# Optimization experiments

Measured on AMD Instinct MI355X. Metric: run time of the kernel, lower is better.

The kernel has to match this reference:

```python
import jax, jax.numpy as jnp
import numpy as np

USER_DIM = 64
ITEM_DIM = 64
HIDDEN = 32
N_USERS = 50000
N_ITEMS = 50000
N_EDGES = 1_600_000


def _xavier_uniform(key, shape):
    fan_in, fan_out = shape[1], shape[0]
    limit = np.sqrt(6.0 / (fan_in + fan_out))
    return jax.random.uniform(key, shape, jnp.float32, -limit, limit)


def setup_inputs() -> dict:
    key = jax.random.key(0)
    k1, k2, k3, k4, k5 = jax.random.split(key, 5)
    user_embeddings = jax.random.normal(k1, (N_USERS, USER_DIM), jnp.float32)
    item_embeddings = jax.random.normal(k2, (N_ITEMS, ITEM_DIM), jnp.float32)
    edge_index = jax.random.randint(k3, (2, N_EDGES), 0, N_USERS, jnp.int64)
    # MLP params: torch Linear weight is [out, in]; xavier_uniform, zero bias
    W1 = _xavier_uniform(k4, (HIDDEN, USER_DIM + ITEM_DIM))
    b1 = jnp.zeros((HIDDEN,), jnp.float32)
    W2 = _xavier_uniform(k5, (1, HIDDEN))
    b2 = jnp.zeros((1,), jnp.float32)
    return {
        "user_embeddings": user_embeddings,
        "item_embeddings": item_embeddings,
        "W1": W1, "b1": b1, "W2": W2, "b2": b2,
        "edge_index": edge_index,
    }


def reference(user_embeddings, item_embeddings, W1, b1, W2, b2, edge_index):
    user_feats = user_embeddings[edge_index[0]]      # [E, user_dim]
    item_feats = item_embeddings[edge_index[1]]      # [E, item_dim]
    edge_feats = jnp.concatenate([user_feats, item_feats], axis=1)  # [E, user_dim+item_dim]
    h = edge_feats @ W1.T + b1                       # [E, 32]
    h = jnp.where(h >= 0, h, 0.2 * h)                # LeakyReLU(0.2)
    logits = h @ W2.T + b2                           # [E, 1]
    return jax.nn.sigmoid(logits).squeeze(-1)        # [E]
```

## Files before the change

kernel.cpp:

```cpp
#include <hip/hip_runtime.h>

typedef unsigned short ushort_t;
typedef __attribute__((ext_vector_type(8))) short short8;
typedef __attribute__((ext_vector_type(4))) float f32x4;
typedef __attribute__((ext_vector_type(2))) _Float16 h2v;
typedef __attribute__((ext_vector_type(4))) _Float16 h4v;

__device__ __forceinline__ ushort_t f2b(float x) {
    unsigned int u = __builtin_bit_cast(unsigned int, x);
    u += 0x7FFFu + ((u >> 16) & 1u);
    return (ushort_t)(u >> 16);
}

__device__ __forceinline__ short8 pack8(const float* __restrict__ p) {
    float4 f0 = *reinterpret_cast<const float4*>(p);
    float4 f1 = *reinterpret_cast<const float4*>(p + 4);
    short8 v;
    v[0] = (short)f2b(f0.x); v[1] = (short)f2b(f0.y);
    v[2] = (short)f2b(f0.z); v[3] = (short)f2b(f0.w);
    v[4] = (short)f2b(f1.x); v[5] = (short)f2b(f1.y);
    v[6] = (short)f2b(f1.z); v[7] = (short)f2b(f1.w);
    return v;
}

__global__ __launch_bounds__(256) void precompute_h(
    const float* __restrict__ ue, const float* __restrict__ ie,
    const float* __restrict__ W1, const float* __restrict__ b1,
    _Float16* __restrict__ hu, _Float16* __restrict__ hi,
    int nu, int ni, int ntu, int ntot)
{
    const int l  = threadIdx.x & 63;
    const int lj = l & 15;
    const int lg = l >> 4;

    int wid = blockIdx.x * (blockDim.x >> 6) + (threadIdx.x >> 6);
    if (wid >= ntot) return;
    const bool isU = wid < ntu;
    const float* tab = isU ? ue : ie;
    _Float16* ht = isU ? hu : hi;
    const int nrows = isU ? nu : ni;
    const int tb   = (isU ? wid : wid - ntu) * 16;
    const int toff = isU ? 0 : 64;

    short8 afrag[2][2];
#pragma unroll
    for (int ks = 0; ks < 2; ++ks)
#pragma unroll
        for (int g = 0; g < 2; ++g)
            afrag[ks][g] = pack8(W1 + (g * 16 + lj) * 128 + toff + ks * 32 + lg * 8);

    int r = tb + lj; if (r >= nrows) r = nrows - 1;
    const float* rp = tab + (long)r * 64;
    short8 bfrag0 = pack8(rp + lg * 8);
    short8 bfrag1 = pack8(rp + 32 + lg * 8);

    f32x4 acc[2];
#pragma unroll
    for (int g = 0; g < 2; ++g)
#pragma unroll
        for (int q = 0; q < 4; ++q)
            acc[g][q] = isU ? b1[g * 16 + lg * 4 + q] : 0.f;

    acc[0] = __builtin_amdgcn_mfma_f32_16x16x32_bf16(afrag[0][0], bfrag0, acc[0], 0, 0, 0);
    acc[1] = __builtin_amdgcn_mfma_f32_16x16x32_bf16(afrag[0][1], bfrag0, acc[1], 0, 0, 0);
    acc[0] = __builtin_amdgcn_mfma_f32_16x16x32_bf16(afrag[1][0], bfrag1, acc[0], 0, 0, 0);
    acc[1] = __builtin_amdgcn_mfma_f32_16x16x32_bf16(afrag[1][1], bfrag1, acc[1], 0, 0, 0);

    if (tb + lj < nrows) {
#pragma unroll
        for (int g = 0; g < 2; ++g) {
            h4v v;
#pragma unroll
            for (int q = 0; q < 4; ++q) v[q] = (_Float16)acc[g][q];
            *reinterpret_cast<h4v*>(ht + (long)r * 32 + g * 16 + lg * 4) = v;
        }
    }
}

#if __has_builtin(__builtin_amdgcn_fdot2)
__device__ __forceinline__ float fdot2(h2v a, h2v b, float c) {
    return __builtin_amdgcn_fdot2(a, b, c, false);
}
#else
__device__ __forceinline__ float fdot2(h2v a, h2v b, float c) {
    return c + (float)a[0] * (float)b[0] + (float)a[1] * (float)b[1];
}
#endif

__global__ __launch_bounds__(256) void edge_final(
    const _Float16* __restrict__ hu, const _Float16* __restrict__ hi,
    const float* __restrict__ w2, const float* __restrict__ b2v,
    const int* __restrict__ idx, float* __restrict__ out,
    long E, long ngroups)
{
    const int l = threadIdx.x & 63;
    const int c = l & 3;
    const int g = l >> 2;

    long wid = (long)blockIdx.x * (blockDim.x >> 6) + (threadIdx.x >> 6);
    if (wid >= ngroups) return;

    h2v w2h[4];
#pragma unroll
    for (int k = 0; k < 4; ++k) {
        w2h[k][0] = (_Float16)w2[c * 8 + 2 * k];
        w2h[k][1] = (_Float16)w2[c * 8 + 2 * k + 1];
    }
    const float bb2 = b2v[0];
    const _Float16 sl = (_Float16)0.2f;
    const h2v slope = {sl, sl};

    long e0 = wid * 64;
    long el = e0 + l; if (el >= E) el = E - 1;
    int uidx = idx[el];
    int iidx = idx[E + el];

    uint4 hur[4], hir[4];
#pragma unroll
    for (int s = 0; s < 4; ++s) {
        int u  = __shfl(uidx, s * 16 + g);
        int it = __shfl(iidx, s * 16 + g);
        hur[s] = *reinterpret_cast<const uint4*>(hu + (long)u  * 32 + c * 8);
        hir[s] = *reinterpret_cast<const uint4*>(hi + (long)it * 32 + c * 8);
    }

    float pt[4];
#pragma unroll
    for (int s = 0; s < 4; ++s) {
        const unsigned int* au = reinterpret_cast<const unsigned int*>(&hur[s]);
        const unsigned int* ai = reinterpret_cast<const unsigned int*>(&hir[s]);
        float p = 0.f;
#pragma unroll
        for (int k = 0; k < 4; ++k) {
            h2v a = __builtin_bit_cast(h2v, au[k]);
            h2v b = __builtin_bit_cast(h2v, ai[k]);
            h2v h = a + b;
            h = __builtin_elementwise_max(h, h * slope);
            p = fdot2(h, w2h[k], p);
        }
        p += __shfl_xor(p, 1);
        p += __shfl_xor(p, 2);
        pt[s] = p;
    }

    int src = (l & 15) * 4;
    float v0 = __shfl(pt[0], src);
    float v1 = __shfl(pt[1], src);
    float v2 = __shfl(pt[2], src);
    float v3 = __shfl(pt[3], src);
    int sr = l >> 4;
    float pv = sr == 0 ? v0 : sr == 1 ? v1 : sr == 2 ? v2 : v3;

    float x = pv + bb2;
    float z = __builtin_amdgcn_exp2f(-1.442695040888963f * x);
    float sig = __builtin_amdgcn_rcpf(1.f + z);
    long eo = e0 + l;
    if (eo < E) out[eo] = sig;
}

__global__ __launch_bounds__(256) void edge_mlp_fp32(
    const float* __restrict__ ue, const float* __restrict__ ie,
    const float* __restrict__ W1, const float* __restrict__ b1,
    const float* __restrict__ w2, const float* __restrict__ b2v,
    const int* __restrict__ idx, float* __restrict__ out, long E)
{
    __shared__ float w1s[128][32];
    for (int t = threadIdx.x; t < 4096; t += blockDim.x) {
        int k = t >> 5, j = t & 31;
        w1s[k][j] = W1[j * 128 + k];
    }
    __syncthreads();
    long e = (long)blockIdx.x * blockDim.x + threadIdx.x;
    if (e >= E) return;
    int u = idx[e], it = idx[E + e];
    const float* ur = ue + (long)u * 64;
    const float* ir = ie + (long)it * 64;
    float acc[32];
#pragma unroll
    for (int j = 0; j < 32; ++j) acc[j] = b1[j];
    for (int k = 0; k < 64; k += 4) {
        float4 f = *reinterpret_cast<const float4*>(ur + k);
        float fv[4] = {f.x, f.y, f.z, f.w};
#pragma unroll
        for (int q = 0; q < 4; ++q)
#pragma unroll
            for (int j = 0; j < 32; ++j) acc[j] += w1s[k + q][j] * fv[q];
    }
    for (int k = 0; k < 64; k += 4) {
        float4 f = *reinterpret_cast<const float4*>(ir + k);
        float fv[4] = {f.x, f.y, f.z, f.w};
#pragma unroll
        for (int q = 0; q < 4; ++q)
#pragma unroll
            for (int j = 0; j < 32; ++j) acc[j] += w1s[64 + k + q][j] * fv[q];
    }
    float lgt = b2v[0];
#pragma unroll
    for (int j = 0; j < 32; ++j) {
        float h = acc[j]; h = h >= 0.f ? h : 0.2f * h;
        lgt += h * w2[j];
    }
    out[e] = 1.0f / (1.0f + expf(-lgt));
}

extern "C" void kernel_launch(void* const* d_in, const int* in_sizes, int n_in,
                              void* d_out, int out_size, void* d_ws, size_t ws_size,
                              hipStream_t stream) {
    const float* ue  = (const float*)d_in[0];
    const float* ie  = (const float*)d_in[1];
    const float* W1  = (const float*)d_in[2];
    const float* b1  = (const float*)d_in[3];
    const float* w2  = (const float*)d_in[4];
    const float* b2v = (const float*)d_in[5];
    const int*   idx = (const int*)d_in[6];
    float* out = (float*)d_out;

    long nu = in_sizes[0] / 64;
    long ni = in_sizes[1] / 64;
    long E  = in_sizes[6] / 2;

    size_t need = (size_t)(nu + ni) * 32 * sizeof(_Float16);
    if (ws_size >= need) {
        _Float16* hu = (_Float16*)d_ws;
        _Float16* hi = hu + (size_t)nu * 32;

        int ntu = (int)((nu + 15) / 16);
        int nti = (int)((ni + 15) / 16);
        int ntot = ntu + nti;
        int pblocks = (ntot + 3) / 4;
        precompute_h<<<pblocks, 256, 0, stream>>>(ue, ie, W1, b1, hu, hi,
                                                  (int)nu, (int)ni, ntu, ntot);

        long ngroups = (E + 63) / 64;
        int mblocks = (int)((ngroups + 3) / 4);
        edge_final<<<mblocks, 256, 0, stream>>>(hu, hi, w2, b2v, idx, out, E, ngroups);
    } else {
        edge_mlp_fp32<<<(int)((E + 255) / 256), 256, 0, stream>>>(
            ue, ie, W1, b1, w2, b2v, idx, out, E);
    }
}
```

Measured before the change: 45.56 us.

## Make edge kernel persistent with software-pipelined prefetch of gathered rows

The edge kernel becomes a grid-stride persistent loop over a fixed grid of 1024 blocks. Each wave prefetches the next group's indices and gathered hidden-vector rows while it computes the current group, hiding gather latency behind compute. The cost is higher register pressure from double-buffered uint4 arrays and fewer resident waves issuing independent loads. With 25000 groups, each wave handles roughly six iterations.

```diff
diff --git a/kernel.cpp b/kernel.cpp
--- a/kernel.cpp
+++ b/kernel.cpp
@@ -98,6 +98,7 @@
     const int g = l >> 2;
 
     long wid = (long)blockIdx.x * (blockDim.x >> 6) + (threadIdx.x >> 6);
+    long nw  = (long)gridDim.x * (blockDim.x >> 6);
     if (wid >= ngroups) return;
 
     h2v w2h[4];
@@ -110,11 +111,13 @@
     const _Float16 sl = (_Float16)0.2f;
     const h2v slope = {sl, sl};
 
-    long e0 = wid * 64;
-    long el = e0 + l; if (el >= E) el = E - 1;
-    int uidx = idx[el];
-    int iidx = idx[E + el];
-
+    long g_cur = wid;
+    int uidx, iidx;
+    {
+        long e = g_cur * 64 + l; if (e >= E) e = E - 1;
+        uidx = idx[e];
+        iidx = idx[E + e];
+    }
     uint4 hur[4], hir[4];
 #pragma unroll
     for (int s = 0; s < 4; ++s) {
@@ -123,39 +126,76 @@
         hur[s] = *reinterpret_cast<const uint4*>(hu + (long)u  * 32 + c * 8);
         hir[s] = *reinterpret_cast<const uint4*>(hi + (long)it * 32 + c * 8);
     }
-
-    float pt[4];
-#pragma unroll
-    for (int s = 0; s < 4; ++s) {
-        const unsigned int* au = reinterpret_cast<const unsigned int*>(&hur[s]);
-        const unsigned int* ai = reinterpret_cast<const unsigned int*>(&hir[s]);
-        float p = 0.f;
-#pragma unroll
-        for (int k = 0; k < 4; ++k) {
-            h2v a = __builtin_bit_cast(h2v, au[k]);
-            h2v b = __builtin_bit_cast(h2v, ai[k]);
-            h2v h = a + b;
-            h = __builtin_elementwise_max(h, h * slope);
-            p = fdot2(h, w2h[k], p);
+    int uidxN, iidxN;
+    {
+        long gn = g_cur + nw;
+        long gs = gn < ngroups ? gn : g_cur;
+        long e = gs * 64 + l; if (e >= E) e = E - 1;
+        uidxN = idx[e];
+        iidxN = idx[E + e];
+    }
+
+    while (true) {
+        long g_next = g_cur + nw;
+        bool have = g_next < ngroups;
+
+        uint4 hurN[4], hirN[4];
+        int uidx2 = uidxN, iidx2 = iidxN;
+        if (have) {
+#pragma unroll
+            for (int s = 0; s < 4; ++s) {
+                int u  = __shfl(uidxN, s * 16 + g);
+                int it = __shfl(iidxN, s * 16 + g);
+                hurN[s] = *reinterpret_cast<const uint4*>(hu + (long)u  * 32 + c * 8);
+                hirN[s] = *reinterpret_cast<const uint4*>(hi + (long)it * 32 + c * 8);
+            }
+            long g2 = g_next + nw;
+            long gs = g2 < ngroups ? g2 : g_next;
+            long e = gs * 64 + l; if (e >= E) e = E - 1;
+            uidx2 = idx[e];
+            iidx2 = idx[E + e];
         }
-        p += __shfl_xor(p, 1);
-        p += __shfl_xor(p, 2);
-        pt[s] = p;
-    }
-
-    int src = (l & 15) * 4;
-    float v0 = __shfl(pt[0], src);
-    float v1 = __shfl(pt[1], src);
-    float v2 = __shfl(pt[2], src);
-    float v3 = __shfl(pt[3], src);
-    int sr = l >> 4;
-    float pv = sr == 0 ? v0 : sr == 1 ? v1 : sr == 2 ? v2 : v3;
-
-    float x = pv + bb2;
-    float z = __builtin_amdgcn_exp2f(-1.442695040888963f * x);
-    float sig = __builtin_amdgcn_rcpf(1.f + z);
-    long eo = e0 + l;
-    if (eo < E) out[eo] = sig;
+
+        long e0 = g_cur * 64;
+        float pt[4];
+#pragma unroll
+        for (int s = 0; s < 4; ++s) {
+            const unsigned int* au = reinterpret_cast<const unsigned int*>(&hur[s]);
+            const unsigned int* ai = reinterpret_cast<const unsigned int*>(&hir[s]);
+            float p = 0.f;
+#pragma unroll
+            for (int k = 0; k < 4; ++k) {
+                h2v a = __builtin_bit_cast(h2v, au[k]);
+                h2v b = __builtin_bit_cast(h2v, ai[k]);
+                h2v h = a + b;
+                h = __builtin_elementwise_max(h, h * slope);
+                p = fdot2(h, w2h[k], p);
+            }
+            p += __shfl_xor(p, 1);
+            p += __shfl_xor(p, 2);
+            pt[s] = p;
+        }
+
+        int src = (l & 15) * 4;
+        float v0 = __shfl(pt[0], src);
+        float v1 = __shfl(pt[1], src);
+        float v2 = __shfl(pt[2], src);
+        float v3 = __shfl(pt[3], src);
+        int sr = l >> 4;
+        float pv = sr == 0 ? v0 : sr == 1 ? v1 : sr == 2 ? v2 : v3;
+
+        float x = pv + bb2;
+        float z = __builtin_amdgcn_exp2f(-1.442695040888963f * x);
+        float sig = __builtin_amdgcn_rcpf(1.f + z);
+        long eo = e0 + l;
+        if (eo < E) out[eo] = sig;
+
+        if (!have) break;
+#pragma unroll
+        for (int s = 0; s < 4; ++s) { hur[s] = hurN[s]; hir[s] = hirN[s]; }
+        uidxN = uidx2; iidxN = iidx2;
+        g_cur = g_next;
+    }
 }
 
 __global__ __launch_bounds__(256) void edge_mlp_fp32(
@@ -232,7 +272,7 @@
                                                   (int)nu, (int)ni, ntu, ntot);
 
         long ngroups = (E + 63) / 64;
-        int mblocks = (int)((ngroups + 3) / 4);
+        int mblocks = 1024;
         edge_final<<<mblocks, 256, 0, stream>>>(hu, hi, w2, b2v, idx, out, E, ngroups);
     } else {
         edge_mlp_fp32<<<(int)((E + 255) / 256), 256, 0, stream>>>(
```

After: 46.48 us. 2.0% more time.

## Quantize precomputed per-node hidden projections to int8 with per-row scales

Applied to the files above, without the earlier changes.

The per-node first-layer projections are now stored as 8-bit values with a per-row float scale instead of fp16, halving the bytes gathered per edge in the edge kernel. To keep the stored projections accurate before quantizing, the precompute splits inputs and weights into bf16 hi/lo parts and runs three MFMAs per product instead of one. The edge kernel dequantizes with FMAs, applies LeakyReLU and the W2 dot in fp32. The cost is an extra random 4-byte scale gather per node lookup, more unpacking ALU work, and int8 quantization error in the logits.

```diff
diff --git a/kernel.cpp b/kernel.cpp
--- a/kernel.cpp
+++ b/kernel.cpp
@@ -3,30 +3,36 @@
 typedef unsigned short ushort_t;
 typedef __attribute__((ext_vector_type(8))) short short8;
 typedef __attribute__((ext_vector_type(4))) float f32x4;
-typedef __attribute__((ext_vector_type(2))) _Float16 h2v;
-typedef __attribute__((ext_vector_type(4))) _Float16 h4v;
 
 __device__ __forceinline__ ushort_t f2b(float x) {
     unsigned int u = __builtin_bit_cast(unsigned int, x);
     u += 0x7FFFu + ((u >> 16) & 1u);
     return (ushort_t)(u >> 16);
 }
-
-__device__ __forceinline__ short8 pack8(const float* __restrict__ p) {
+__device__ __forceinline__ float b2f(ushort_t b) {
+    unsigned int u = ((unsigned int)b) << 16;
+    return __builtin_bit_cast(float, u);
+}
+
+__device__ __forceinline__ void pack_pair(const float* __restrict__ p,
+                                          short8& hi, short8& lo) {
     float4 f0 = *reinterpret_cast<const float4*>(p);
     float4 f1 = *reinterpret_cast<const float4*>(p + 4);
-    short8 v;
-    v[0] = (short)f2b(f0.x); v[1] = (short)f2b(f0.y);
-    v[2] = (short)f2b(f0.z); v[3] = (short)f2b(f0.w);
-    v[4] = (short)f2b(f1.x); v[5] = (short)f2b(f1.y);
-    v[6] = (short)f2b(f1.z); v[7] = (short)f2b(f1.w);
-    return v;
-}
-
-__global__ __launch_bounds__(256) void precompute_h(
+    float f[8] = {f0.x, f0.y, f0.z, f0.w, f1.x, f1.y, f1.z, f1.w};
+#pragma unroll
+    for (int e = 0; e < 8; ++e) {
+        ushort_t hb = f2b(f[e]);
+        hi[e] = (short)hb;
+        float r = f[e] - b2f(hb);
+        lo[e] = (short)f2b(r);
+    }
+}
+
+__global__ __launch_bounds__(256) void precompute_q8(
     const float* __restrict__ ue, const float* __restrict__ ie,
     const float* __restrict__ W1, const float* __restrict__ b1,
-    _Float16* __restrict__ hu, _Float16* __restrict__ hi,
+    unsigned char* __restrict__ um, unsigned char* __restrict__ im,
+    float* __restrict__ usc, float* __restrict__ isc,
     int nu, int ni, int ntu, int ntot)
 {
     const int l  = threadIdx.x & 63;
@@ -37,22 +43,25 @@
     if (wid >= ntot) return;
     const bool isU = wid < ntu;
     const float* tab = isU ? ue : ie;
-    _Float16* ht = isU ? hu : hi;
+    unsigned char* mant = isU ? um : im;
+    float* sc = isU ? usc : isc;
     const int nrows = isU ? nu : ni;
     const int tb   = (isU ? wid : wid - ntu) * 16;
     const int toff = isU ? 0 : 64;
 
-    short8 afrag[2][2];
+    short8 ahi[2][2], alo[2][2];
 #pragma unroll
     for (int ks = 0; ks < 2; ++ks)
 #pragma unroll
         for (int g = 0; g < 2; ++g)
-            afrag[ks][g] = pack8(W1 + (g * 16 + lj) * 128 + toff + ks * 32 + lg * 8);
+            pack_pair(W1 + (g * 16 + lj) * 128 + toff + ks * 32 + lg * 8,
+                      ahi[ks][g], alo[ks][g]);
 
     int r = tb + lj; if (r >= nrows) r = nrows - 1;
     const float* rp = tab + (long)r * 64;
-    short8 bfrag0 = pack8(rp + lg * 8);
-    short8 bfrag1 = pack8(rp + 32 + lg * 8);
+    short8 bhi0, blo0, bhi1, blo1;
+    pack_pair(rp + lg * 8,      bhi0, blo0);
+    pack_pair(rp + 32 + lg * 8, bhi1, blo1);
 
     f32x4 acc[2];
 #pragma unroll
@@ -61,34 +70,46 @@
         for (int q = 0; q < 4; ++q)
             acc[g][q] = isU ? b1[g * 16 + lg * 4 + q] : 0.f;
 
-    acc[0] = __builtin_amdgcn_mfma_f32_16x16x32_bf16(afrag[0][0], bfrag0, acc[0], 0, 0, 0);
-    acc[1] = __builtin_amdgcn_mfma_f32_16x16x32_bf16(afrag[0][1], bfrag0, acc[1], 0, 0, 0);
-    acc[0] = __builtin_amdgcn_mfma_f32_16x16x32_bf16(afrag[1][0], bfrag1, acc[0], 0, 0, 0);
-    acc[1] = __builtin_amdgcn_mfma_f32_16x16x32_bf16(afrag[1][1], bfrag1, acc[1], 0, 0, 0);
+#pragma unroll
+    for (int g = 0; g < 2; ++g) {
+        acc[g] = __builtin_amdgcn_mfma_f32_16x16x32_bf16(ahi[0][g], bhi0, acc[g], 0, 0, 0);
+        acc[g] = __builtin_amdgcn_mfma_f32_16x16x32_bf16(ahi[0][g], blo0, acc[g], 0, 0, 0);
+        acc[g] = __builtin_amdgcn_mfma_f32_16x16x32_bf16(alo[0][g], bhi0, acc[g], 0, 0, 0);
+        acc[g] = __builtin_amdgcn_mfma_f32_16x16x32_bf16(ahi[1][g], bhi1, acc[g], 0, 0, 0);
+        acc[g] = __builtin_amdgcn_mfma_f32_16x16x32_bf16(ahi[1][g], blo1, acc[g], 0, 0, 0);
+        acc[g] = __builtin_amdgcn_mfma_f32_16x16x32_bf16(alo[1][g], bhi1, acc[g], 0, 0, 0);
+    }
+
+    float m = 0.f;
+#pragma unroll
+    for (int g = 0; g < 2; ++g)
+#pragma unroll
+        for (int q = 0; q < 4; ++q)
+            m = fmaxf(m, fabsf(acc[g][q]));
+    m = fmaxf(m, __shfl_xor(m, 16));
+    m = fmaxf(m, __shfl_xor(m, 32));
+    float inv = m > 0.f ? 127.f / m : 0.f;
 
     if (tb + lj < nrows) {
 #pragma unroll
         for (int g = 0; g < 2; ++g) {
-            h4v v;
-#pragma unroll
-            for (int q = 0; q < 4; ++q) v[q] = (_Float16)acc[g][q];
-            *reinterpret_cast<h4v*>(ht + (long)r * 32 + g * 16 + lg * 4) = v;
+            unsigned int w = 0;
+#pragma unroll
+            for (int q = 0; q < 4; ++q) {
+                float qf = __builtin_rintf(acc[g][q] * inv);
+                qf = fminf(fmaxf(qf, -127.f), 127.f);
+                int qi = (int)qf + 128;
+                w |= ((unsigned int)qi & 0xFFu) << (8 * q);
+            }
+            *reinterpret_cast<unsigned int*>(mant + (long)r * 32 + g * 16 + lg * 4) = w;
         }
-    }
-}
-
-#if __has_builtin(__builtin_amdgcn_fdot2)
-__device__ __forceinline__ float fdot2(h2v a, h2v b, float c) {
-    return __builtin_amdgcn_fdot2(a, b, c, false);
-}
-#else
-__device__ __forceinline__ float fdot2(h2v a, h2v b, float c) {
-    return c + (float)a[0] * (float)b[0] + (float)a[1] * (float)b[1];
-}
-#endif
-
-__global__ __launch_bounds__(256) void edge_final(
-    const _Float16* __restrict__ hu, const _Float16* __restrict__ hi,
+        if (lg == 0) sc[r] = m * (1.f / 127.f);
+    }
+}
+
+__global__ __launch_bounds__(256) void edge_final_q8(
+    const unsigned char* __restrict__ um, const unsigned char* __restrict__ im,
+    const float* __restrict__ usc, const float* __restrict__ isc,
     const float* __restrict__ w2, const float* __restrict__ b2v,
     const int* __restrict__ idx, float* __restrict__ out,
     long E, long ngroups)
@@ -100,43 +121,51 @@
     long wid = (long)blockIdx.x * (blockDim.x >> 6) + (threadIdx.x >> 6);
     if (wid >= ngroups) return;
 
-    h2v w2h[4];
-#pragma unroll
-    for (int k = 0; k < 4; ++k) {
-        w2h[k][0] = (_Float16)w2[c * 8 + 2 * k];
-        w2h[k][1] = (_Float16)w2[c * 8 + 2 * k + 1];
-    }
+    float w2v[8];
+#pragma unroll
+    for (int q = 0; q < 8; ++q) w2v[q] = w2[c * 8 + q];
     const float bb2 = b2v[0];
-    const _Float16 sl = (_Float16)0.2f;
-    const h2v slope = {sl, sl};
 
     long e0 = wid * 64;
     long el = e0 + l; if (el >= E) el = E - 1;
     int uidx = idx[el];
     int iidx = idx[E + el];
 
-    uint4 hur[4], hir[4];
+    uint2 mu[4], mi[4];
+    float su[4], si[4];
 #pragma unroll
     for (int s = 0; s < 4; ++s) {
         int u  = __shfl(uidx, s * 16 + g);
         int it = __shfl(iidx, s * 16 + g);
-        hur[s] = *reinterpret_cast<const uint4*>(hu + (long)u  * 32 + c * 8);
-        hir[s] = *reinterpret_cast<const uint4*>(hi + (long)it * 32 + c * 8);
+        mu[s] = *reinterpret_cast<const uint2*>(um + (long)u  * 32 + c * 8);
+        mi[s] = *reinterpret_cast<const uint2*>(im + (long)it * 32 + c * 8);
+        su[s] = usc[u];
+        si[s] = isc[it];
     }
 
     float pt[4];
 #pragma unroll
     for (int s = 0; s < 4; ++s) {
-        const unsigned int* au = reinterpret_cast<const unsigned int*>(&hur[s]);
-        const unsigned int* ai = reinterpret_cast<const unsigned int*>(&hir[s]);
+        const float a = su[s], b = si[s];
+        const float off = -128.f * (a + b);
         float p = 0.f;
-#pragma unroll
-        for (int k = 0; k < 4; ++k) {
-            h2v a = __builtin_bit_cast(h2v, au[k]);
-            h2v b = __builtin_bit_cast(h2v, ai[k]);
-            h2v h = a + b;
-            h = __builtin_elementwise_max(h, h * slope);
-            p = fdot2(h, w2h[k], p);
+        unsigned int wu = mu[s].x, wi = mi[s].x;
+#pragma unroll
+        for (int q = 0; q < 4; ++q) {
+            float fu = (float)((wu >> (8 * q)) & 0xFFu);
+            float fi = (float)((wi >> (8 * q)) & 0xFFu);
+            float h = fmaf(b, fi, fmaf(a, fu, off));
+            h = fmaxf(h, 0.2f * h);
+            p = fmaf(h, w2v[q], p);
+        }
+        wu = mu[s].y; wi = mi[s].y;
+#pragma unroll
+        for (int q = 0; q < 4; ++q) {
+            float fu = (float)((wu >> (8 * q)) & 0xFFu);
+            float fi = (float)((wi >> (8 * q)) & 0xFFu);
+            float h = fmaf(b, fi, fmaf(a, fu, off));
+            h = fmaxf(h, 0.2f * h);
+            p = fmaf(h, w2v[4 + q], p);
         }
         p += __shfl_xor(p, 1);
         p += __shfl_xor(p, 2);
@@ -219,21 +248,24 @@
     long ni = in_sizes[1] / 64;
     long E  = in_sizes[6] / 2;
 
-    size_t need = (size_t)(nu + ni) * 32 * sizeof(_Float16);
+    size_t need = (size_t)(nu + ni) * 32 + (size_t)(nu + ni) * 4;
     if (ws_size >= need) {
-        _Float16* hu = (_Float16*)d_ws;
-        _Float16* hi = hu + (size_t)nu * 32;
+        unsigned char* um = (unsigned char*)d_ws;
+        unsigned char* im = um + (size_t)nu * 32;
+        float* usc = (float*)(im + (size_t)ni * 32);
+        float* isc = usc + nu;
 
         int ntu = (int)((nu + 15) / 16);
         int nti = (int)((ni + 15) / 16);
         int ntot = ntu + nti;
         int pblocks = (ntot + 3) / 4;
-        precompute_h<<<pblocks, 256, 0, stream>>>(ue, ie, W1, b1, hu, hi,
-                                                  (int)nu, (int)ni, ntu, ntot);
+        precompute_q8<<<pblocks, 256, 0, stream>>>(ue, ie, W1, b1, um, im, usc, isc,
+                                                   (int)nu, (int)ni, ntu, ntot);
 
         long ngroups = (E + 63) / 64;
         int mblocks = (int)((ngroups + 3) / 4);
-        edge_final<<<mblocks, 256, 0, stream>>>(hu, hi, w2, b2v, idx, out, E, ngroups);
+        edge_final_q8<<<mblocks, 256, 0, stream>>>(um, im, usc, isc, w2, b2v,
+                                                   idx, out, E, ngroups);
     } else {
         edge_mlp_fp32<<<(int)((E + 255) / 256), 256, 0, stream>>>(
             ue, ie, W1, b1, w2, b2v, idx, out, E);
```

After: 48.77 us. 7.0% more time.
